# Performance work log

Measured on AMD Instinct MI355X. Metric: run time of the kernel, lower is better.

The kernel has to match this reference:

```python
import jax, jax.numpy as jnp
import numpy as np
import math

H = 12  # heads (init kwarg)
KEEP_RATE = 0.7  # forward arg keep_rate (< 1 -> token pruning path)


def setup_inputs() -> dict:
    key = jax.random.key(0)
    k0, k1, k2 = jax.random.split(key, 3)
    b, n, c = 32, 577, 768  # ViT-B/16 @ 384px: 576 patches + CLS
    x = jax.random.normal(k0, (b, n, c), dtype=jnp.float32)
    # nn.Linear(dim, dim*3) and nn.Linear(dim, dim); kaiming-ish scale
    W_qkv = jax.random.normal(k1, (c, 3 * c), dtype=jnp.float32) / np.sqrt(c).astype(np.float32)
    b_qkv = jnp.zeros((3 * c,), dtype=jnp.float32)
    W_out = jax.random.normal(k2, (c, c), dtype=jnp.float32) / np.sqrt(c).astype(np.float32)
    b_out = jnp.zeros((c,), dtype=jnp.float32)
    return {"x": x, "keep_rate": KEEP_RATE, "W_qkv": W_qkv, "b_qkv": b_qkv,
            "W_out": W_out, "b_out": b_out}


def reference(x, keep_rate, W_qkv, b_qkv, W_out, b_out):
    b, n, c = x.shape
    d = c // H
    scale = (c / H) ** -0.5
    # qkv projection + split into heads: 'b n (h d) -> b h n d'
    qkv = x @ W_qkv + b_qkv                      # [b, n, 3c]
    q, k, v = jnp.split(qkv, 3, axis=-1)
    split_heads = lambda t: t.reshape(b, n, H, d).transpose(0, 2, 1, 3)
    q, k, v = split_heads(q), split_heads(k), split_heads(v)
    dots = jnp.einsum('bhid,bhjd->bhij', q, k) * scale   # [b,h,n,n]
    attention = jax.nn.softmax(dots, axis=-1)
    out = jnp.einsum('bhij,bhjd->bhid', attention, v)    # [b,h,n,d]
    out = out.transpose(0, 2, 1, 3).reshape(b, n, c)     # 'b h n d -> b n (h d)'
    out = out @ W_out + b_out                            # to_out (dropout=0)
    final_tokens = n - 1
    if keep_rate < 1:
        final_tokens = math.ceil(keep_rate * final_tokens)
        # CLS-token attention to patch tokens, averaged over heads
        class_attention = attention[:, :, 0, 1:].mean(axis=1)   # [b, n-1]
        _, ind = jax.lax.top_k(class_attention, final_tokens)    # [b, final_tokens]
        ind = jnp.sort(ind, axis=1)
        index = jnp.broadcast_to(ind[:, :, None], (b, final_tokens, c))
        return (x, index, ind, class_attention, final_tokens)
    return (out, None, None, None, final_tokens)
```

## Files before the change

### kernel.cpp

```cpp
#include <hip/hip_runtime.h>
#include <hip/hip_bf16.h>
#include <math.h>

#define BATCH 32
#define NTOK 577
#define NPATCH 576
#define CDIM 768
#define HEADS 12
#define DHEAD 64
#define W3 2304
#define FT 404

#define WS_QCLS  0
#define WS_WTIL  24576
#define WS_DBIAS 319488
#define WS_DOTS  319872
#define WS_IND   541440
#define WS_CA    554368

#define O_X      0ULL
#define O_INDEX  14180352ULL
#define O_IND    24109056ULL
#define O_CA     24121984ULL
#define O_FT     24140416ULL

__global__ __launch_bounds__(256) void k_qcls(const float* __restrict__ x,
                                              const float* __restrict__ W,
                                              const float* __restrict__ bias,
                                              float* __restrict__ qcls) {
    __shared__ float xs[CDIM];
    const int b = blockIdx.x, chunk = blockIdx.y, tid = threadIdx.x;
    for (int i = tid; i < CDIM; i += 256) xs[i] = x[(size_t)b * NTOK * CDIM + i];
    __syncthreads();
    const int col = chunk * 256 + tid;
    float a0 = 0.f, a1 = 0.f, a2 = 0.f, a3 = 0.f;
    for (int c = 0; c < CDIM; c += 4) {
        a0 += xs[c]     * W[(size_t)c * W3 + col];
        a1 += xs[c + 1] * W[(size_t)(c + 1) * W3 + col];
        a2 += xs[c + 2] * W[(size_t)(c + 2) * W3 + col];
        a3 += xs[c + 3] * W[(size_t)(c + 3) * W3 + col];
    }
    qcls[b * CDIM + col] = (a0 + a1) + (a2 + a3) + bias[col];
}

__global__ __launch_bounds__(256) void k_wtil(const float* __restrict__ W,
                                              const float* __restrict__ bias,
                                              const float* __restrict__ qcls,
                                              float* __restrict__ wtil,
                                              float* __restrict__ dbias) {
    __shared__ float qs[DHEAD];
    const int b = blockIdx.x, h = blockIdx.y, tid = threadIdx.x;
    if (tid < DHEAD) qs[tid] = qcls[b * CDIM + h * DHEAD + tid];
    __syncthreads();
    if (tid < 64) {
        float t = qs[tid] * bias[CDIM + h * DHEAD + tid];
        #pragma unroll
        for (int off = 32; off; off >>= 1) t += __shfl_down(t, off);
        if (tid == 0) dbias[b * HEADS + h] = t;
    }
    for (int c = tid; c < CDIM; c += 256) {
        const float* wr = W + (size_t)c * W3 + CDIM + h * DHEAD;
        float acc = 0.f;
        #pragma unroll
        for (int d = 0; d < DHEAD; d += 4) {
            float4 a = *reinterpret_cast<const float4*>(wr + d);
            acc += a.x * qs[d] + a.y * qs[d + 1] + a.z * qs[d + 2] + a.w * qs[d + 3];
        }
        wtil[((size_t)b * HEADS + h) * CDIM + c] = acc;
    }
}

__global__ __launch_bounds__(256) void k_dots(const float* __restrict__ x,
                                              const float* __restrict__ wtil,
                                              const float* __restrict__ dbias,
                                              float* __restrict__ dots,
                                              float* __restrict__ out0) {
    __shared__ float wt[HEADS * CDIM];
    __shared__ float db[HEADS];
    const int b = blockIdx.x, tid = threadIdx.x;
    for (int i = tid; i < HEADS * CDIM; i += 256) wt[i] = wtil[(size_t)b * HEADS * CDIM + i];
    if (tid < HEADS) db[tid] = dbias[b * HEADS + tid];
    __syncthreads();
    const int wave = tid >> 6, lane = tid & 63;
    for (int it = 0; it < 8; it++) {
        const int j = blockIdx.y * 32 + it * 4 + wave;
        if (j >= NTOK) break;
        const float4* xp = reinterpret_cast<const float4*>(x + ((size_t)b * NTOK + j) * CDIM);
        float4* op = reinterpret_cast<float4*>(out0 + ((size_t)b * NTOK + j) * CDIM);
        float acc[HEADS];
        #pragma unroll
        for (int h = 0; h < HEADS; h++) acc[h] = 0.f;
        #pragma unroll
        for (int i = 0; i < 3; i++) {
            float4 a = xp[i * 64 + lane];
            op[i * 64 + lane] = a;
            const int cbase = i * 256 + lane * 4;
            #pragma unroll
            for (int h = 0; h < HEADS; h++) {
                float4 w = *reinterpret_cast<const float4*>(&wt[h * CDIM + cbase]);
                acc[h] += a.x * w.x + a.y * w.y + a.z * w.z + a.w * w.w;
            }
        }
        #pragma unroll
        for (int off = 32; off; off >>= 1)
            #pragma unroll
            for (int h = 0; h < HEADS; h++) acc[h] += __shfl_down(acc[h], off);
        if (lane == 0) {
            #pragma unroll
            for (int h = 0; h < HEADS; h++)
                dots[((size_t)b * HEADS + h) * NTOK + j] = 0.125f * (acc[h] + db[h]);
        }
    }
}

__global__ __launch_bounds__(256) void k_softmax(const float* __restrict__ dots,
                                                 float* __restrict__ ca_f32,
                                                 float* __restrict__ out3) {
    __shared__ float dl[HEADS * NTOK];
    __shared__ float red[256];
    __shared__ float mh[HEADS], sh[HEADS];
    const int b = blockIdx.x, tid = threadIdx.x;
    for (int i = tid; i < HEADS * NTOK; i += 256) dl[i] = dots[(size_t)b * HEADS * NTOK + i];
    __syncthreads();
    for (int h = 0; h < HEADS; h++) {
        float m = -3.4e38f;
        for (int j = tid; j < NTOK; j += 256) m = fmaxf(m, dl[h * NTOK + j]);
        red[tid] = m; __syncthreads();
        for (int s = 128; s; s >>= 1) { if (tid < s) red[tid] = fmaxf(red[tid], red[tid + s]); __syncthreads(); }
        const float mm = red[0]; __syncthreads();
        float sum = 0.f;
        for (int j = tid; j < NTOK; j += 256) sum += expf(dl[h * NTOK + j] - mm);
        red[tid] = sum; __syncthreads();
        for (int s = 128; s; s >>= 1) { if (tid < s) red[tid] += red[tid + s]; __syncthreads(); }
        if (tid == 0) { mh[h] = mm; sh[h] = red[0]; }
        __syncthreads();
    }
    for (int j = 1 + tid; j < NTOK; j += 256) {
        float ca = 0.f;
        #pragma unroll
        for (int h = 0; h < HEADS; h++) ca += expf(dl[h * NTOK + j] - mh[h]) / sh[h];
        ca *= (1.f / 12.f);
        ca_f32[b * NPATCH + (j - 1)] = ca;
        out3[(size_t)b * NPATCH + (j - 1)] = ca;
    }
}

__global__ __launch_bounds__(576) void k_topk(const float* __restrict__ ca,
                                              int* __restrict__ ind_ws,
                                              float* __restrict__ out2,
                                              float* __restrict__ out4,
                                              int write_ft) {
    __shared__ unsigned int vals[NPATCH];
    __shared__ int flags[NPATCH];
    const int b = blockIdx.x, tid = threadIdx.x;
    const unsigned int myv = __float_as_uint(ca[b * NPATCH + tid]);
    vals[tid] = myv;
    __syncthreads();
    int rank = 0;
    for (int j = 0; j < NPATCH; j++) {
        const unsigned int v = vals[j];
        rank += (v > myv) || (v == myv && j < tid);
    }
    flags[tid] = (rank < FT) ? 1 : 0;
    __syncthreads();
    if (flags[tid]) {
        int pos = 0;
        for (int j = 0; j < NPATCH; j++) pos += (j < tid) ? flags[j] : 0;
        ind_ws[b * FT + pos] = tid;
        out2[(size_t)b * FT + pos] = (float)tid;
    }
    if (b == 0 && tid == 0 && write_ft) out4[0] = (float)FT;
}

__global__ __launch_bounds__(256) void k_bcast(const int* __restrict__ ind,
                                               float* __restrict__ out1) {
    const unsigned int g = blockIdx.x * 256u + threadIdx.x;
    const unsigned int e = g * 4u;
    const unsigned int row = e / CDIM;
    const float v = (float)ind[row];
    float4 o; o.x = v; o.y = v; o.z = v; o.w = v;
    *reinterpret_cast<float4*>(out1 + e) = o;
}

extern "C" void kernel_launch(void* const* d_in, const int* in_sizes, int n_in,
                              void* d_out, int out_size, void* d_ws, size_t ws_size,
                              hipStream_t stream) {
    const float* x  = (const float*)d_in[0];
    const float* W  = (const float*)d_in[2];
    const float* bq = (const float*)d_in[3];
    float* ws = (float*)d_ws;
    float* out = (float*)d_out;

    k_qcls<<<dim3(BATCH, 3), 256, 0, stream>>>(x, W, bq, ws + WS_QCLS);
    k_wtil<<<dim3(BATCH, HEADS), 256, 0, stream>>>(W, bq, ws + WS_QCLS, ws + WS_WTIL, ws + WS_DBIAS);
    k_dots<<<dim3(BATCH, 19), 256, 0, stream>>>(x, ws + WS_WTIL, ws + WS_DBIAS, ws + WS_DOTS, out + O_X);
    k_softmax<<<BATCH, 256, 0, stream>>>(ws + WS_DOTS, ws + WS_CA, out + O_CA);
    const int write_ft = (out_size > (int)O_FT) ? 1 : 0;
    k_topk<<<BATCH, 576, 0, stream>>>(ws + WS_CA, (int*)(ws + WS_IND), out + O_IND, out + O_FT, write_ft);
    k_bcast<<<9696, 256, 0, stream>>>((const int*)(ws + WS_IND), out + O_INDEX);
}
```

Baseline: 270.8 us.

## Fuse CLS query into fold kernel and softmax with top-k selection

Computes the CLS query projection inside the per-head fold kernel, so the separate q_cls kernel and its workspace round-trip go away. Softmax, class-attention averaging and rank-based top-k now run in one 768-thread kernel that uses one wave per head with shuffle reductions instead of sequential per-head block reductions. This cuts two launches and several barrier-heavy reduction loops. In exchange, each (b,h) block recomputes its own 64 q values, which is no extra total work, but the per-column strided W reads may coalesce less well.

```diff
diff --git a/kernel.cpp b/kernel.cpp
--- a/kernel.cpp
+++ b/kernel.cpp
@@ -11,12 +11,10 @@
 #define W3 2304
 #define FT 404
 
-#define WS_QCLS  0
 #define WS_WTIL  24576
 #define WS_DBIAS 319488
 #define WS_DOTS  319872
 #define WS_IND   541440
-#define WS_CA    554368
 
 #define O_X      0ULL
 #define O_INDEX  14180352ULL
@@ -24,40 +22,38 @@
 #define O_CA     24121984ULL
 #define O_FT     24140416ULL
 
-__global__ __launch_bounds__(256) void k_qcls(const float* __restrict__ x,
+__global__ __launch_bounds__(256) void k_fold(const float* __restrict__ x,
                                               const float* __restrict__ W,
                                               const float* __restrict__ bias,
-                                              float* __restrict__ qcls) {
-    __shared__ float xs[CDIM];
-    const int b = blockIdx.x, chunk = blockIdx.y, tid = threadIdx.x;
-    for (int i = tid; i < CDIM; i += 256) xs[i] = x[(size_t)b * NTOK * CDIM + i];
-    __syncthreads();
-    const int col = chunk * 256 + tid;
-    float a0 = 0.f, a1 = 0.f, a2 = 0.f, a3 = 0.f;
-    for (int c = 0; c < CDIM; c += 4) {
-        a0 += xs[c]     * W[(size_t)c * W3 + col];
-        a1 += xs[c + 1] * W[(size_t)(c + 1) * W3 + col];
-        a2 += xs[c + 2] * W[(size_t)(c + 2) * W3 + col];
-        a3 += xs[c + 3] * W[(size_t)(c + 3) * W3 + col];
-    }
-    qcls[b * CDIM + col] = (a0 + a1) + (a2 + a3) + bias[col];
-}
-
-__global__ __launch_bounds__(256) void k_wtil(const float* __restrict__ W,
-                                              const float* __restrict__ bias,
-                                              const float* __restrict__ qcls,
                                               float* __restrict__ wtil,
                                               float* __restrict__ dbias) {
+    __shared__ float x0s[CDIM];
+    __shared__ float red[256];
     __shared__ float qs[DHEAD];
     const int b = blockIdx.x, h = blockIdx.y, tid = threadIdx.x;
-    if (tid < DHEAD) qs[tid] = qcls[b * CDIM + h * DHEAD + tid];
+    for (int i = tid; i < CDIM; i += 256) x0s[i] = x[(size_t)b * NTOK * CDIM + i];
     __syncthreads();
-    if (tid < 64) {
-        float t = qs[tid] * bias[CDIM + h * DHEAD + tid];
+    {
+        const int d = tid & 63, seg = tid >> 6;
+        const float* Wq = W + (size_t)(h * DHEAD + d);
+        float acc = 0.f;
+        const int c0 = seg * 192;
+        #pragma unroll 8
+        for (int c = c0; c < c0 + 192; c++)
+            acc += x0s[c] * Wq[(size_t)c * W3];
+        red[tid] = acc;
+    }
+    __syncthreads();
+    if (tid < DHEAD) {
+        float q = red[tid] + red[tid + 64] + red[tid + 128] + red[tid + 192]
+                + bias[h * DHEAD + tid];
+        qs[tid] = q;
+        float t = q * bias[CDIM + h * DHEAD + tid];
         #pragma unroll
         for (int off = 32; off; off >>= 1) t += __shfl_down(t, off);
         if (tid == 0) dbias[b * HEADS + h] = t;
     }
+    __syncthreads();
     for (int c = tid; c < CDIM; c += 256) {
         const float* wr = W + (size_t)c * W3 + CDIM + h * DHEAD;
         float acc = 0.f;
@@ -104,7 +100,7 @@
         #pragma unroll
         for (int off = 32; off; off >>= 1)
             #pragma unroll
-            for (int h = 0; h < HEADS; h++) acc[h] += __shfl_down(acc[h], off);
+            for (int h = 0; h < HEADS; h++) acc[h] += __shfl_xor(acc[h], off);
         if (lane == 0) {
             #pragma unroll
             for (int h = 0; h < HEADS; h++)
@@ -113,63 +109,60 @@
     }
 }
 
-__global__ __launch_bounds__(256) void k_softmax(const float* __restrict__ dots,
-                                                 float* __restrict__ ca_f32,
-                                                 float* __restrict__ out3) {
+__global__ __launch_bounds__(768) void k_catopk(const float* __restrict__ dots,
+                                                float* __restrict__ ca_out,
+                                                float* __restrict__ ind_out,
+                                                float* __restrict__ ft_out,
+                                                int* __restrict__ ind_ws,
+                                                int write_ft) {
     __shared__ float dl[HEADS * NTOK];
-    __shared__ float red[256];
     __shared__ float mh[HEADS], sh[HEADS];
-    const int b = blockIdx.x, tid = threadIdx.x;
-    for (int i = tid; i < HEADS * NTOK; i += 256) dl[i] = dots[(size_t)b * HEADS * NTOK + i];
-    __syncthreads();
-    for (int h = 0; h < HEADS; h++) {
-        float m = -3.4e38f;
-        for (int j = tid; j < NTOK; j += 256) m = fmaxf(m, dl[h * NTOK + j]);
-        red[tid] = m; __syncthreads();
-        for (int s = 128; s; s >>= 1) { if (tid < s) red[tid] = fmaxf(red[tid], red[tid + s]); __syncthreads(); }
-        const float mm = red[0]; __syncthreads();
-        float sum = 0.f;
-        for (int j = tid; j < NTOK; j += 256) sum += expf(dl[h * NTOK + j] - mm);
-        red[tid] = sum; __syncthreads();
-        for (int s = 128; s; s >>= 1) { if (tid < s) red[tid] += red[tid + s]; __syncthreads(); }
-        if (tid == 0) { mh[h] = mm; sh[h] = red[0]; }
-        __syncthreads();
-    }
-    for (int j = 1 + tid; j < NTOK; j += 256) {
-        float ca = 0.f;
-        #pragma unroll
-        for (int h = 0; h < HEADS; h++) ca += expf(dl[h * NTOK + j] - mh[h]) / sh[h];
-        ca *= (1.f / 12.f);
-        ca_f32[b * NPATCH + (j - 1)] = ca;
-        out3[(size_t)b * NPATCH + (j - 1)] = ca;
-    }
-}
-
-__global__ __launch_bounds__(576) void k_topk(const float* __restrict__ ca,
-                                              int* __restrict__ ind_ws,
-                                              float* __restrict__ out2,
-                                              float* __restrict__ out4,
-                                              int write_ft) {
     __shared__ unsigned int vals[NPATCH];
     __shared__ int flags[NPATCH];
     const int b = blockIdx.x, tid = threadIdx.x;
-    const unsigned int myv = __float_as_uint(ca[b * NPATCH + tid]);
-    vals[tid] = myv;
+    for (int i = tid; i < HEADS * NTOK; i += 768) dl[i] = dots[(size_t)b * HEADS * NTOK + i];
     __syncthreads();
-    int rank = 0;
-    for (int j = 0; j < NPATCH; j++) {
-        const unsigned int v = vals[j];
-        rank += (v > myv) || (v == myv && j < tid);
+    {
+        const int w = tid >> 6, lane = tid & 63;
+        const float* row = dl + w * NTOK;
+        float m = -3.4e38f;
+        for (int j = lane; j < NTOK; j += 64) m = fmaxf(m, row[j]);
+        #pragma unroll
+        for (int off = 32; off; off >>= 1) m = fmaxf(m, __shfl_xor(m, off));
+        float s = 0.f;
+        for (int j = lane; j < NTOK; j += 64) s += expf(row[j] - m);
+        #pragma unroll
+        for (int off = 32; off; off >>= 1) s += __shfl_xor(s, off);
+        if (lane == 0) { mh[w] = m; sh[w] = s; }
     }
-    flags[tid] = (rank < FT) ? 1 : 0;
     __syncthreads();
-    if (flags[tid]) {
+    if (tid < NPATCH) {
+        float ca = 0.f;
+        #pragma unroll
+        for (int h = 0; h < HEADS; h++)
+            ca += expf(dl[h * NTOK + 1 + tid] - mh[h]) / sh[h];
+        ca *= (1.f / 12.f);
+        ca_out[(size_t)b * NPATCH + tid] = ca;
+        vals[tid] = __float_as_uint(ca);
+    }
+    __syncthreads();
+    if (tid < NPATCH) {
+        const unsigned int myv = vals[tid];
+        int rank = 0;
+        for (int j = 0; j < NPATCH; j++) {
+            const unsigned int v = vals[j];
+            rank += (v > myv) || (v == myv && j < tid);
+        }
+        flags[tid] = (rank < FT) ? 1 : 0;
+    }
+    __syncthreads();
+    if (tid < NPATCH && flags[tid]) {
         int pos = 0;
-        for (int j = 0; j < NPATCH; j++) pos += (j < tid) ? flags[j] : 0;
+        for (int j = 0; j < tid; j++) pos += flags[j];
         ind_ws[b * FT + pos] = tid;
-        out2[(size_t)b * FT + pos] = (float)tid;
+        ind_out[(size_t)b * FT + pos] = (float)tid;
     }
-    if (b == 0 && tid == 0 && write_ft) out4[0] = (float)FT;
+    if (b == 0 && tid == 0 && write_ft) ft_out[0] = (float)FT;
 }
 
 __global__ __launch_bounds__(256) void k_bcast(const int* __restrict__ ind,
@@ -191,11 +184,10 @@
     float* ws = (float*)d_ws;
     float* out = (float*)d_out;
 
-    k_qcls<<<dim3(BATCH, 3), 256, 0, stream>>>(x, W, bq, ws + WS_QCLS);
-    k_wtil<<<dim3(BATCH, HEADS), 256, 0, stream>>>(W, bq, ws + WS_QCLS, ws + WS_WTIL, ws + WS_DBIAS);
+    k_fold<<<dim3(BATCH, HEADS), 256, 0, stream>>>(x, W, bq, ws + WS_WTIL, ws + WS_DBIAS);
     k_dots<<<dim3(BATCH, 19), 256, 0, stream>>>(x, ws + WS_WTIL, ws + WS_DBIAS, ws + WS_DOTS, out + O_X);
-    k_softmax<<<BATCH, 256, 0, stream>>>(ws + WS_DOTS, ws + WS_CA, out + O_CA);
     const int write_ft = (out_size > (int)O_FT) ? 1 : 0;
-    k_topk<<<BATCH, 576, 0, stream>>>(ws + WS_CA, (int*)(ws + WS_IND), out + O_IND, out + O_FT, write_ft);
+    k_catopk<<<BATCH, 768, 0, stream>>>(ws + WS_DOTS, out + O_CA, out + O_IND, out + O_FT,
+                                        (int*)(ws + WS_IND), write_ft);
     k_bcast<<<9696, 256, 0, stream>>>((const int*)(ws + WS_IND), out + O_INDEX);
 }
```

Result: faster. 226.1 us (-16.5%).
